# Kernel optimization log

Hardware: AMD Instinct MI355X
Metric: run time of the kernel (lower is better)

## Reference

```python
import jax, jax.numpy as jnp
import numpy as np

EMBED_DIM = 1024
NUM_HEADS = 16
HEAD_DIM = EMBED_DIM // NUM_HEADS
EPSILON = 1e-6
SCORE_SCALE = 1.0
B, L = 2, 2048


def setup_inputs() -> dict:
    key = jax.random.key(0)
    k0, k1, k2, k3, k4 = jax.random.split(key, 5)
    s_in = 1.0 / np.sqrt(EMBED_DIM)
    return {
        "x": jax.random.normal(k0, (B, L, EMBED_DIM), dtype=jnp.float32),
        "w_qkv": jax.random.normal(k1, (EMBED_DIM, 3 * EMBED_DIM), dtype=jnp.float32) * s_in,
        "b_qkv": jnp.zeros((3 * EMBED_DIM,), dtype=jnp.float32),
        "w_out": jax.random.normal(k2, (EMBED_DIM, EMBED_DIM), dtype=jnp.float32) * s_in,
        "b_out": jnp.zeros((EMBED_DIM,), dtype=jnp.float32),
    }


def reference(x, w_qkv, b_qkv, w_out, b_out):
    Bq, Lq, E = x.shape
    qkv = x @ w_qkv + b_qkv  # [B, L, 3E]
    q, k, v = jnp.split(qkv, 3, axis=-1)
    q = q.reshape(Bq, Lq, NUM_HEADS, HEAD_DIM).transpose(0, 2, 1, 3)  # bhld
    k = k.reshape(Bq, Lq, NUM_HEADS, HEAD_DIM).transpose(0, 2, 1, 3)
    v = v.reshape(Bq, Lq, NUM_HEADS, HEAD_DIM).transpose(0, 2, 1, 3)

    dot = jnp.einsum('bhid,bhjd->bhij', q, k)
    q_norm_sq = jnp.sum(q * q, axis=-1, keepdims=True)          # [b,h,L,1]
    k_norm_sq = jnp.sum(k * k, axis=-1, keepdims=True)          # [b,h,L,1]
    vals = q_norm_sq + k_norm_sq.transpose(0, 1, 3, 2)          # [b,h,L,L]
    scores = (dot * dot) / (vals - 2.0 * dot + EPSILON) * SCORE_SCALE

    mask = jnp.triu(jnp.ones((Lq, Lq), dtype=scores.dtype), k=1) * -1e9
    scores = scores + mask[None, None, :, :]
    attn = jax.nn.softmax(scores, axis=-1)
    out = jnp.einsum('bhij,bhjd->bhid', attn, v)
    out = out.transpose(0, 2, 1, 3).reshape(Bq, Lq, E)
    return out @ w_out + b_out
```

## Files before the change

kernel.cpp:

```cpp
#include <hip/hip_runtime.h>

#define EMBED 1024
#define NH 16
#define HD 64
#define SEQ 2048
#define BATCH 2
#define ROWS (BATCH*SEQ)
#define BHD (BATCH*NH)

typedef __bf16 bf16x8 __attribute__((ext_vector_type(8)));
typedef _Float16 f16x4 __attribute__((ext_vector_type(4)));
typedef float f32x4 __attribute__((ext_vector_type(4)));

__device__ __forceinline__ unsigned short f2bf(float f){
  union { float f; unsigned u; } v; v.f = f;
  unsigned r = v.u + 0x7fffu + ((v.u >> 16) & 1u);
  return (unsigned short)(r >> 16);
}
__device__ __forceinline__ float bf2f(unsigned short s){
  union { unsigned u; float f; } v; v.u = ((unsigned)s) << 16; return v.f;
}
__device__ __forceinline__ unsigned short f2h(float f){
  union { _Float16 h; unsigned short u; } v; v.h = (_Float16)f; return v.u;
}

typedef __attribute__((address_space(1))) unsigned int as1_t;
typedef __attribute__((address_space(3))) unsigned int as3_t;
__device__ __forceinline__ void async_ld16(const void* gp, void* lp){
  __builtin_amdgcn_global_load_lds((as1_t*)gp, (as3_t*)lp, 16, 0, 0);
}


__global__ __launch_bounds__(256) void k_prep(
    const float* __restrict__ x,     unsigned short* __restrict__ xb,
    const float* __restrict__ wqkv,  unsigned short* __restrict__ wqkvT,
    const float* __restrict__ wout,  unsigned short* __restrict__ woutT)
{
  __shared__ float t[32][33];
  int tid = threadIdx.x;
  int bx = blockIdx.x;
  if (bx < 4096){
    int i = bx*256 + tid;
    float4 f = ((const float4*)x)[i];
    ushort4 o; o.x=f2bf(f.x); o.y=f2bf(f.y); o.z=f2bf(f.z); o.w=f2bf(f.w);
    ((ushort4*)xb)[i] = o;
    return;
  }
  const float* in; unsigned short* out; int R, C, c0, r0;
  if (bx < 4096 + 3072){
    int bid = bx - 4096;
    in = wqkv; out = wqkvT; R = 1024; C = 3072;
    c0 = (bid % 96) * 32; r0 = (bid / 96) * 32;
  } else {
    int bid = bx - 7168;
    in = wout; out = woutT; R = 1024; C = 1024;
    c0 = (bid & 31) * 32; r0 = (bid >> 5) * 32;
  }
  int tx = tid & 31, ty = tid >> 5;
  #pragma unroll
  for (int i = 0; i < 4; i++){ int r = ty + i*8; t[r][tx] = in[(size_t)(r0+r)*C + c0 + tx]; }
  __syncthreads();
  #pragma unroll
  for (int i = 0; i < 4; i++){ int rr = ty + i*8; out[(size_t)(c0+rr)*R + r0 + tx] = f2bf(t[tx][rr]); }
}


__global__ __launch_bounds__(256) void k_gemm_qkv(
    const unsigned short* __restrict__ A,
    const unsigned short* __restrict__ BT,
    const float* __restrict__ bias,
    unsigned short* __restrict__ qo, unsigned short* __restrict__ ko,
    unsigned short* __restrict__ vT,
    float* __restrict__ qn, float* __restrict__ kn)
{
  __shared__ __align__(16) unsigned short As[128*32];
  __shared__ __align__(16) unsigned short Bs[128*32];
  const int K = EMBED;
  int m0 = blockIdx.x * 128, n0 = blockIdx.y * 128;
  int tid = threadIdx.x, lane = tid & 63, wave = tid >> 6;
  int wm = wave >> 1, wn = wave & 1;
  int l16 = lane & 15, quad = lane >> 4;
  f32x4 acc[4][4] = {};
  int c0i = wave*64 + lane, c1i = 256 + wave*64 + lane;
  int r0 = c0i >> 2, cc0 = (c0i & 3) * 8;
  int r1 = c1i >> 2, cc1 = (c1i & 3) * 8;
  unsigned short* lA0 = &As[(wave*64)*8];
  unsigned short* lA1 = &As[(256 + wave*64)*8];
  unsigned short* lB0 = &Bs[(wave*64)*8];
  unsigned short* lB1 = &Bs[(256 + wave*64)*8];
  for (int k0 = 0; k0 < K; k0 += 32){
    async_ld16((void*)&A [(size_t)(m0 + r0)*K + k0 + cc0], (void*)lA0);
    async_ld16((void*)&A [(size_t)(m0 + r1)*K + k0 + cc1], (void*)lA1);
    async_ld16((void*)&BT[(size_t)(n0 + r0)*K + k0 + cc0], (void*)lB0);
    async_ld16((void*)&BT[(size_t)(n0 + r1)*K + k0 + cc1], (void*)lB1);
    __syncthreads();
    bf16x8 af[4], bfr[4];
    #pragma unroll
    for (int mi = 0; mi < 4; mi++) af[mi]  = *(const bf16x8*)&As[(wm*64 + mi*16 + l16)*32 + quad*8];
    #pragma unroll
    for (int ni = 0; ni < 4; ni++) bfr[ni] = *(const bf16x8*)&Bs[(wn*64 + ni*16 + l16)*32 + quad*8];
    #pragma unroll
    for (int mi = 0; mi < 4; mi++)
      #pragma unroll
      for (int ni = 0; ni < 4; ni++)
        acc[mi][ni] = __builtin_amdgcn_mfma_f32_16x16x32_bf16(af[mi], bfr[ni], acc[mi][ni], 0, 0, 0);
    __syncthreads();
  }

  int which = n0 >> 10;
  int h = ((n0 & 1023) >> 6) + wn;
  if (which < 2){
    unsigned short* dst = (which == 0) ? qo : ko;
    float* ndst = (which == 0) ? qn : kn;
    #pragma unroll
    for (int mi = 0; mi < 4; mi++){
      float ns[4] = {0.f, 0.f, 0.f, 0.f};
      #pragma unroll
      for (int ni = 0; ni < 4; ni++)
        #pragma unroll
        for (int rr = 0; rr < 4; rr++){
          int row = m0 + wm*64 + mi*16 + quad*4 + rr;
          int col = n0 + wn*64 + ni*16 + l16;
          unsigned short bits = f2bf(acc[mi][ni][rr] + bias[col]);
          int b = row >> 11, l = row & 2047;
          dst[(((size_t)(b*NH + h))*SEQ + l)*HD + (col & 63)] = bits;
          float vq = bf2f(bits);
          ns[rr] += vq * vq;
        }
      #pragma unroll
      for (int rr = 0; rr < 4; rr++){
        float s = ns[rr];
        s += __shfl_xor(s, 1); s += __shfl_xor(s, 2);
        s += __shfl_xor(s, 4); s += __shfl_xor(s, 8);
        if (l16 == 0){
          int row = m0 + wm*64 + mi*16 + quad*4 + rr;
          int b = row >> 11, l = row & 2047;
          ndst[(size_t)(b*NH + h)*SEQ + l] = s;
        }
      }
    }
  } else {
    #pragma unroll
    for (int mi = 0; mi < 4; mi++)
      #pragma unroll
      for (int ni = 0; ni < 4; ni++){
        int row0 = m0 + wm*64 + mi*16 + quad*4;
        int col = n0 + wn*64 + ni*16 + l16;
        int b = row0 >> 11, l0 = row0 & 2047;
        ushort4 pk; unsigned short* pks = (unsigned short*)&pk;
        #pragma unroll
        for (int rr = 0; rr < 4; rr++)
          pks[rr] = f2h(acc[mi][ni][rr] + bias[col]);
        *(ushort4*)&vT[(((size_t)(b*NH + h))*HD + (col & 63))*SEQ + l0] = pk;
      }
  }
}


__global__ __launch_bounds__(128, 4) void k_attn(
    const unsigned short* __restrict__ qg,
    const unsigned short* __restrict__ kg,
    const unsigned short* __restrict__ vtg,
    const float* __restrict__ qn,
    const float* __restrict__ kn,
    float* __restrict__ Opart,
    float* __restrict__ Mp,
    float* __restrict__ Lp)
{
  __shared__ __align__(16) unsigned short Ks[2][32*72];
  __shared__ __align__(16) _Float16      Vs[2][64*36];
  int bh = blockIdx.y;
  int tid = threadIdx.x, lane = tid & 63, wave = tid >> 6;
  int l16 = lane & 15, quad = lane >> 4;
  int P = blockIdx.x >> 1, s = blockIdx.x & 1;

  const unsigned short* qbase = qg  + (size_t)bh * SEQ * HD;
  const unsigned short* kbase = kg  + (size_t)bh * SEQ * HD;
  const _Float16*       vtb   = (const _Float16*)vtg + (size_t)bh * HD * SEQ;
  const float* knb = kn + (size_t)bh * SEQ;

  int kd0 = tid >> 3,         kc0 = tid & 7;
  int kd1 = (tid + 128) >> 3, kc1 = tid & 7;
  int vd0 = tid >> 2,         vc0 = tid & 3;
  int vd1 = 32 + (tid >> 2),  vc1 = tid & 3;

  #pragma unroll
  for (int pass = 0; pass < 2; pass++){
    int t = pass ? (63 - P) : P;
    int nj = t + 1;
    int half = (nj + 1) >> 1;
    int jb_lo = s ? half : 0;
    int jb_hi = s ? nj : half;
    int q0 = t*32 + wave*16;

    bf16x8 aq[2];
    #pragma unroll
    for (int sk = 0; sk < 2; sk++)
      aq[sk] = *(const bf16x8*)&qbase[(size_t)(q0 + l16)*HD + sk*32 + quad*8];
    float qn_m = qn[(size_t)bh*SEQ + q0 + l16];

    float m_run = -1e30f, l_lane = 0.f;
    f32x4 oacc[4] = {};

    if (jb_lo < jb_hi){
      int jlo = jb_lo * 32;
      {
        uint4 ka = *(const uint4*)&kbase[(size_t)(jlo + kd0)*HD + kc0*8];
        uint4 kb = *(const uint4*)&kbase[(size_t)(jlo + kd1)*HD + kc1*8];
        uint4 va = *(const uint4*)&vtb[(size_t)vd0*SEQ + jlo + vc0*8];
        uint4 vb = *(const uint4*)&vtb[(size_t)vd1*SEQ + jlo + vc1*8];
        *(uint4*)&Ks[0][kd0*72 + kc0*8] = ka;
        *(uint4*)&Ks[0][kd1*72 + kc1*8] = kb;
        *(uint2*)&Vs[0][vd0*36 + vc0*8]     = make_uint2(va.x, va.y);
        *(uint2*)&Vs[0][vd0*36 + vc0*8 + 4] = make_uint2(va.z, va.w);
        *(uint2*)&Vs[0][vd1*36 + vc1*8]     = make_uint2(vb.x, vb.y);
        *(uint2*)&Vs[0][vd1*36 + vc1*8 + 4] = make_uint2(vb.z, vb.w);
      }
      __syncthreads();

      for (int jb = jb_lo; jb < jb_hi; jb++){
        int j0 = jb * 32;
        int buf = (jb - jb_lo) & 1;
        int jn = (jb + 1 < jb_hi) ? (jb + 1)*32 : j0;
        uint4 ka = *(const uint4*)&kbase[(size_t)(jn + kd0)*HD + kc0*8];
        uint4 kb = *(const uint4*)&kbase[(size_t)(jn + kd1)*HD + kc1*8];
        uint4 va = *(const uint4*)&vtb[(size_t)vd0*SEQ + jn + vc0*8];
        uint4 vb = *(const uint4*)&vtb[(size_t)vd1*SEQ + jn + vc1*8];

        f32x4 st[2] = {};
        #pragma unroll
        for (int tile = 0; tile < 2; tile++)
          #pragma unroll
          for (int sk = 0; sk < 2; sk++){
            bf16x8 ak = *(const bf16x8*)&Ks[buf][(tile*16 + l16)*72 + (sk*4 + quad)*8];
            st[tile] = __builtin_amdgcn_mfma_f32_16x16x32_bf16(ak, aq[sk], st[tile], 0, 0, 0);
          }
        float4 kn_a = *(const float4*)&knb[j0 + quad*4];
        float4 kn_b = *(const float4*)&knb[j0 + 16 + quad*4];
        float kn_j[2][4] = {{kn_a.x, kn_a.y, kn_a.z, kn_a.w}, {kn_b.x, kn_b.y, kn_b.z, kn_b.w}};
        int mg = q0 + l16;
        float sc[2][4];
        if (j0 + 32 > q0){
          #pragma unroll
          for (int tile = 0; tile < 2; tile++)
            #pragma unroll
            for (int rr = 0; rr < 4; rr++){
              int jg = j0 + tile*16 + quad*4 + rr;
              float dot = st[tile][rr];
              float den = fmaxf(qn_m + kn_j[tile][rr] - 2.0f*dot, 0.0f) + 1e-6f;
              float v = dot * dot * __builtin_amdgcn_rcpf(den);
              sc[tile][rr] = (jg <= mg) ? v : -1e30f;
            }
        } else {
          #pragma unroll
          for (int tile = 0; tile < 2; tile++)
            #pragma unroll
            for (int rr = 0; rr < 4; rr++){
              float dot = st[tile][rr];
              float den = fmaxf(qn_m + kn_j[tile][rr] - 2.0f*dot, 0.0f) + 1e-6f;
              sc[tile][rr] = dot * dot * __builtin_amdgcn_rcpf(den);
            }
        }
        float mx = fmaxf(fmaxf(fmaxf(sc[0][0], sc[0][1]), fmaxf(sc[0][2], sc[0][3])),
                         fmaxf(fmaxf(sc[1][0], sc[1][1]), fmaxf(sc[1][2], sc[1][3])));
        mx = fmaxf(mx, __shfl_xor(mx, 16));
        mx = fmaxf(mx, __shfl_xor(mx, 32));
        float mnew = fmaxf(m_run, mx);
        float alpha = __expf(m_run - mnew);
        m_run = mnew;

        float ps = 0.f;
        #pragma unroll
        for (int tile = 0; tile < 2; tile++)
          #pragma unroll
          for (int rr = 0; rr < 4; rr++){
            float e = __expf(sc[tile][rr] - mnew);
            sc[tile][rr] = e; ps += e;
          }
        l_lane = l_lane * alpha + ps;

        #pragma unroll
        for (int g = 0; g < 4; g++)
          #pragma unroll
          for (int rr = 0; rr < 4; rr++) oacc[g][rr] *= alpha;

        #pragma unroll
        for (int tile = 0; tile < 2; tile++){
          f16x4 pf;
          #pragma unroll
          for (int rr = 0; rr < 4; rr++) pf[rr] = (_Float16)sc[tile][rr];
          #pragma unroll
          for (int g = 0; g < 4; g++){
            f16x4 av = *(const f16x4*)&Vs[buf][(g*16 + l16)*36 + (tile*4 + quad)*4];
            oacc[g] = __builtin_amdgcn_mfma_f32_16x16x16f16(av, pf, oacc[g], 0, 0, 0);
          }
        }

        *(uint4*)&Ks[buf^1][kd0*72 + kc0*8] = ka;
        *(uint4*)&Ks[buf^1][kd1*72 + kc1*8] = kb;
        *(uint2*)&Vs[buf^1][vd0*36 + vc0*8]     = make_uint2(va.x, va.y);
        *(uint2*)&Vs[buf^1][vd0*36 + vc0*8 + 4] = make_uint2(va.z, va.w);
        *(uint2*)&Vs[buf^1][vd1*36 + vc1*8]     = make_uint2(vb.x, vb.y);
        *(uint2*)&Vs[buf^1][vd1*36 + vc1*8 + 4] = make_uint2(vb.z, vb.w);
        __syncthreads();
      }
    }

    float l_tot = l_lane + __shfl_xor(l_lane, 16);
    l_tot += __shfl_xor(l_tot, 32);

    int r = wave*16 + l16;
    size_t pb = ((size_t)(bh*64 + t)*2 + s) * (32*64);
    #pragma unroll
    for (int g = 0; g < 4; g++){
      float4 pk = make_float4(oacc[g][0], oacc[g][1], oacc[g][2], oacc[g][3]);
      *(float4*)&Opart[pb + (size_t)r*64 + g*16 + quad*4] = pk;
    }
    if (quad == 0){
      int mb = ((bh*64 + t)*2 + s)*32 + r;
      Mp[mb] = m_run;
      Lp[mb] = l_tot;
    }
    __syncthreads();
  }
}


__global__ __launch_bounds__(256) void k_combine(
    const float* __restrict__ Opart,
    const float* __restrict__ Mp,
    const float* __restrict__ Lp,
    unsigned short* __restrict__ attn_out)
{
  int t = blockIdx.x;
  int bh = blockIdx.y; int b = bh >> 4, h = bh & 15;
  int tid = threadIdx.x;
  int d = tid & 63, r8 = (tid >> 6) * 8;
  size_t i0 = ((size_t)(bh*64 + t)*2) * 2048;
  size_t i1 = i0 + 2048;
  int mb = ((bh*64 + t)*2) * 32;
  #pragma unroll
  for (int rr = 0; rr < 8; rr++){
    int r = r8 + rr;
    float m0 = Mp[mb + r],      m1 = Mp[mb + 32 + r];
    float l0 = Lp[mb + r],      l1 = Lp[mb + 32 + r];
    float ms = fmaxf(m0, m1);
    float w0 = __expf(m0 - ms), w1 = __expf(m1 - ms);
    float den = w0*l0 + w1*l1;
    float o = (w0*Opart[i0 + (size_t)r*64 + d] + w1*Opart[i1 + (size_t)r*64 + d]) / den;
    attn_out[(size_t)(b*SEQ + t*32 + r)*EMBED + h*HD + d] = f2bf(o);
  }
}


__global__ __launch_bounds__(256) void k_gemm_out(
    const unsigned short* __restrict__ A,
    const unsigned short* __restrict__ BT,
    const float* __restrict__ bias,
    float* __restrict__ out)
{
  __shared__ __align__(16) unsigned short As[128*32];
  __shared__ __align__(16) unsigned short Bs[128*32];
  const int K = EMBED;
  int m0 = blockIdx.x * 128, n0 = blockIdx.y * 128;
  int tid = threadIdx.x, lane = tid & 63, wave = tid >> 6;
  int wm = wave >> 1, wn = wave & 1;
  int l16 = lane & 15, quad = lane >> 4;
  f32x4 acc[4][4] = {};
  int c0i = wave*64 + lane, c1i = 256 + wave*64 + lane;
  int r0 = c0i >> 2, cc0 = (c0i & 3) * 8;
  int r1 = c1i >> 2, cc1 = (c1i & 3) * 8;
  unsigned short* lA0 = &As[(wave*64)*8];
  unsigned short* lA1 = &As[(256 + wave*64)*8];
  unsigned short* lB0 = &Bs[(wave*64)*8];
  unsigned short* lB1 = &Bs[(256 + wave*64)*8];
  for (int k0 = 0; k0 < K; k0 += 32){
    async_ld16((void*)&A [(size_t)(m0 + r0)*K + k0 + cc0], (void*)lA0);
    async_ld16((void*)&A [(size_t)(m0 + r1)*K + k0 + cc1], (void*)lA1);
    async_ld16((void*)&BT[(size_t)(n0 + r0)*K + k0 + cc0], (void*)lB0);
    async_ld16((void*)&BT[(size_t)(n0 + r1)*K + k0 + cc1], (void*)lB1);
    __syncthreads();
    bf16x8 af[4], bfr[4];
    #pragma unroll
    for (int mi = 0; mi < 4; mi++) af[mi]  = *(const bf16x8*)&As[(wm*64 + mi*16 + l16)*32 + quad*8];
    #pragma unroll
    for (int ni = 0; ni < 4; ni++) bfr[ni] = *(const bf16x8*)&Bs[(wn*64 + ni*16 + l16)*32 + quad*8];
    #pragma unroll
    for (int mi = 0; mi < 4; mi++)
      #pragma unroll
      for (int ni = 0; ni < 4; ni++)
        acc[mi][ni] = __builtin_amdgcn_mfma_f32_16x16x32_bf16(af[mi], bfr[ni], acc[mi][ni], 0, 0, 0);
    __syncthreads();
  }
  #pragma unroll
  for (int mi = 0; mi < 4; mi++)
    #pragma unroll
    for (int ni = 0; ni < 4; ni++)
      #pragma unroll
      for (int rr = 0; rr < 4; rr++){
        int row = m0 + wm*64 + mi*16 + quad*4 + rr;
        int col = n0 + wn*64 + ni*16 + l16;
        out[(size_t)row*EMBED + col] = acc[mi][ni][rr] + bias[col];
      }
}


extern "C" void kernel_launch(void* const* d_in, const int* in_sizes, int n_in,
                              void* d_out, int out_size, void* d_ws, size_t ws_size,
                              hipStream_t stream) {
  const float* x     = (const float*)d_in[0];
  const float* w_qkv = (const float*)d_in[1];
  const float* b_qkv = (const float*)d_in[2];
  const float* w_out = (const float*)d_in[3];
  const float* b_out = (const float*)d_in[4];
  float* out = (float*)d_out;

  char* ws = (char*)d_ws;
  size_t off = 0;
  auto alloc = [&](size_t bytes) -> void* {
    void* p = ws + off; off += (bytes + 255) & ~(size_t)255; return p;
  };
  unsigned short* xb    = (unsigned short*)alloc((size_t)ROWS * EMBED * 2);
  unsigned short* wqkvT = (unsigned short*)alloc((size_t)3 * EMBED * EMBED * 2);
  unsigned short* woutT = (unsigned short*)alloc((size_t)EMBED * EMBED * 2);
  unsigned short* qb    = (unsigned short*)alloc((size_t)ROWS * EMBED * 2);
  unsigned short* kb    = (unsigned short*)alloc((size_t)ROWS * EMBED * 2);
  unsigned short* vTb   = (unsigned short*)alloc((size_t)ROWS * EMBED * 2);
  float* qn = (float*)alloc((size_t)BHD * SEQ * 4);
  float* kn = (float*)alloc((size_t)BHD * SEQ * 4);
  float* Opart = (float*)alloc((size_t)BHD * 64 * 2 * 32 * 64 * 4);
  float* Mp    = (float*)alloc((size_t)BHD * 64 * 2 * 32 * 4);
  float* Lp    = (float*)alloc((size_t)BHD * 64 * 2 * 32 * 4);
  unsigned short* attnb = xb;

  k_prep<<<dim3(4096 + 3072 + 1024), dim3(256), 0, stream>>>(x, xb, w_qkv, wqkvT, w_out, woutT);
  k_gemm_qkv<<<dim3(ROWS/128, 3*EMBED/128), dim3(256), 0, stream>>>(xb, wqkvT, b_qkv, qb, kb, vTb, qn, kn);
  k_attn<<<dim3(64, BHD), dim3(128), 0, stream>>>(qb, kb, vTb, qn, kn, Opart, Mp, Lp);
  k_combine<<<dim3(64, BHD), dim3(256), 0, stream>>>(Opart, Mp, Lp, attnb);
  k_gemm_out<<<dim3(ROWS/128, EMBED/128), dim3(256), 0, stream>>>(attnb, woutT, b_out, out);
}
```

Before: 222.4 us.

## Recompute q norms in attention, store fp16 partials, shrink out-GEMM M tile

```diff
diff --git a/kernel.cpp b/kernel.cpp
--- a/kernel.cpp
+++ b/kernel.cpp
@@ -71,7 +71,7 @@
     const float* __restrict__ bias,
     unsigned short* __restrict__ qo, unsigned short* __restrict__ ko,
     unsigned short* __restrict__ vT,
-    float* __restrict__ qn, float* __restrict__ kn)
+    float* __restrict__ kn)
 {
   __shared__ __align__(16) unsigned short As[128*32];
   __shared__ __align__(16) unsigned short Bs[128*32];
@@ -109,9 +109,19 @@
 
   int which = n0 >> 10;
   int h = ((n0 & 1023) >> 6) + wn;
-  if (which < 2){
-    unsigned short* dst = (which == 0) ? qo : ko;
-    float* ndst = (which == 0) ? qn : kn;
+  if (which == 0){
+    #pragma unroll
+    for (int mi = 0; mi < 4; mi++)
+      #pragma unroll
+      for (int ni = 0; ni < 4; ni++)
+        #pragma unroll
+        for (int rr = 0; rr < 4; rr++){
+          int row = m0 + wm*64 + mi*16 + quad*4 + rr;
+          int col = n0 + wn*64 + ni*16 + l16;
+          int b = row >> 11, l = row & 2047;
+          qo[(((size_t)(b*NH + h))*SEQ + l)*HD + (col & 63)] = f2bf(acc[mi][ni][rr] + bias[col]);
+        }
+  } else if (which == 1){
     #pragma unroll
     for (int mi = 0; mi < 4; mi++){
       float ns[4] = {0.f, 0.f, 0.f, 0.f};
@@ -123,7 +133,7 @@
           int col = n0 + wn*64 + ni*16 + l16;
           unsigned short bits = f2bf(acc[mi][ni][rr] + bias[col]);
           int b = row >> 11, l = row & 2047;
-          dst[(((size_t)(b*NH + h))*SEQ + l)*HD + (col & 63)] = bits;
+          ko[(((size_t)(b*NH + h))*SEQ + l)*HD + (col & 63)] = bits;
           float vq = bf2f(bits);
           ns[rr] += vq * vq;
         }
@@ -135,7 +145,7 @@
         if (l16 == 0){
           int row = m0 + wm*64 + mi*16 + quad*4 + rr;
           int b = row >> 11, l = row & 2047;
-          ndst[(size_t)(b*NH + h)*SEQ + l] = s;
+          kn[(size_t)(b*NH + h)*SEQ + l] = s;
         }
       }
     }
@@ -161,9 +171,8 @@
     const unsigned short* __restrict__ qg,
     const unsigned short* __restrict__ kg,
     const unsigned short* __restrict__ vtg,
-    const float* __restrict__ qn,
     const float* __restrict__ kn,
-    float* __restrict__ Opart,
+    _Float16* __restrict__ Opart,
     float* __restrict__ Mp,
     float* __restrict__ Lp)
 {
@@ -197,7 +206,16 @@
     #pragma unroll
     for (int sk = 0; sk < 2; sk++)
       aq[sk] = *(const bf16x8*)&qbase[(size_t)(q0 + l16)*HD + sk*32 + quad*8];
-    float qn_m = qn[(size_t)bh*SEQ + q0 + l16];
+    float qn_lane = 0.f;
+    #pragma unroll
+    for (int sk = 0; sk < 2; sk++)
+      #pragma unroll
+      for (int i = 0; i < 8; i++){
+        float v = (float)aq[sk][i];
+        qn_lane += v * v;
+      }
+    float qn_m = qn_lane + __shfl_xor(qn_lane, 16);
+    qn_m += __shfl_xor(qn_m, 32);
 
     float m_run = -1e30f, l_lane = 0.f;
     f32x4 oacc[4] = {};
@@ -313,8 +331,10 @@
     size_t pb = ((size_t)(bh*64 + t)*2 + s) * (32*64);
     #pragma unroll
     for (int g = 0; g < 4; g++){
-      float4 pk = make_float4(oacc[g][0], oacc[g][1], oacc[g][2], oacc[g][3]);
-      *(float4*)&Opart[pb + (size_t)r*64 + g*16 + quad*4] = pk;
+      ushort4 pk;
+      pk.x = f2h(oacc[g][0]); pk.y = f2h(oacc[g][1]);
+      pk.z = f2h(oacc[g][2]); pk.w = f2h(oacc[g][3]);
+      *(ushort4*)&Opart[pb + (size_t)r*64 + g*16 + quad*4] = pk;
     }
     if (quad == 0){
       int mb = ((bh*64 + t)*2 + s)*32 + r;
@@ -327,7 +347,7 @@
 
 
 __global__ __launch_bounds__(256) void k_combine(
-    const float* __restrict__ Opart,
+    const _Float16* __restrict__ Opart,
     const float* __restrict__ Mp,
     const float* __restrict__ Lp,
     unsigned short* __restrict__ attn_out)
@@ -347,7 +367,7 @@
     float ms = fmaxf(m0, m1);
     float w0 = __expf(m0 - ms), w1 = __expf(m1 - ms);
     float den = w0*l0 + w1*l1;
-    float o = (w0*Opart[i0 + (size_t)r*64 + d] + w1*Opart[i1 + (size_t)r*64 + d]) / den;
+    float o = (w0*(float)Opart[i0 + (size_t)r*64 + d] + w1*(float)Opart[i1 + (size_t)r*64 + d]) / den;
     attn_out[(size_t)(b*SEQ + t*32 + r)*EMBED + h*HD + d] = f2bf(o);
   }
 }
@@ -359,46 +379,45 @@
     const float* __restrict__ bias,
     float* __restrict__ out)
 {
-  __shared__ __align__(16) unsigned short As[128*32];
+  __shared__ __align__(16) unsigned short As[64*32];
   __shared__ __align__(16) unsigned short Bs[128*32];
   const int K = EMBED;
-  int m0 = blockIdx.x * 128, n0 = blockIdx.y * 128;
+  int m0 = blockIdx.x * 64, n0 = blockIdx.y * 128;
   int tid = threadIdx.x, lane = tid & 63, wave = tid >> 6;
   int wm = wave >> 1, wn = wave & 1;
   int l16 = lane & 15, quad = lane >> 4;
-  f32x4 acc[4][4] = {};
+  f32x4 acc[2][4] = {};
+  int ra = tid >> 2, ca = (tid & 3) * 8;
   int c0i = wave*64 + lane, c1i = 256 + wave*64 + lane;
-  int r0 = c0i >> 2, cc0 = (c0i & 3) * 8;
-  int r1 = c1i >> 2, cc1 = (c1i & 3) * 8;
-  unsigned short* lA0 = &As[(wave*64)*8];
-  unsigned short* lA1 = &As[(256 + wave*64)*8];
+  int rb0 = c0i >> 2, cb0 = (c0i & 3) * 8;
+  int rb1 = c1i >> 2, cb1 = (c1i & 3) * 8;
+  unsigned short* lA  = &As[(wave*64)*8];
   unsigned short* lB0 = &Bs[(wave*64)*8];
   unsigned short* lB1 = &Bs[(256 + wave*64)*8];
   for (int k0 = 0; k0 < K; k0 += 32){
-    async_ld16((void*)&A [(size_t)(m0 + r0)*K + k0 + cc0], (void*)lA0);
-    async_ld16((void*)&A [(size_t)(m0 + r1)*K + k0 + cc1], (void*)lA1);
-    async_ld16((void*)&BT[(size_t)(n0 + r0)*K + k0 + cc0], (void*)lB0);
-    async_ld16((void*)&BT[(size_t)(n0 + r1)*K + k0 + cc1], (void*)lB1);
+    async_ld16((void*)&A [(size_t)(m0 + ra)*K + k0 + ca],   (void*)lA);
+    async_ld16((void*)&BT[(size_t)(n0 + rb0)*K + k0 + cb0], (void*)lB0);
+    async_ld16((void*)&BT[(size_t)(n0 + rb1)*K + k0 + cb1], (void*)lB1);
     __syncthreads();
-    bf16x8 af[4], bfr[4];
-    #pragma unroll
-    for (int mi = 0; mi < 4; mi++) af[mi]  = *(const bf16x8*)&As[(wm*64 + mi*16 + l16)*32 + quad*8];
+    bf16x8 af[2], bfr[4];
+    #pragma unroll
+    for (int mi = 0; mi < 2; mi++) af[mi]  = *(const bf16x8*)&As[(wm*32 + mi*16 + l16)*32 + quad*8];
     #pragma unroll
     for (int ni = 0; ni < 4; ni++) bfr[ni] = *(const bf16x8*)&Bs[(wn*64 + ni*16 + l16)*32 + quad*8];
     #pragma unroll
-    for (int mi = 0; mi < 4; mi++)
+    for (int mi = 0; mi < 2; mi++)
       #pragma unroll
       for (int ni = 0; ni < 4; ni++)
         acc[mi][ni] = __builtin_amdgcn_mfma_f32_16x16x32_bf16(af[mi], bfr[ni], acc[mi][ni], 0, 0, 0);
     __syncthreads();
   }
   #pragma unroll
-  for (int mi = 0; mi < 4; mi++)
+  for (int mi = 0; mi < 2; mi++)
     #pragma unroll
     for (int ni = 0; ni < 4; ni++)
       #pragma unroll
       for (int rr = 0; rr < 4; rr++){
-        int row = m0 + wm*64 + mi*16 + quad*4 + rr;
+        int row = m0 + wm*32 + mi*16 + quad*4 + rr;
         int col = n0 + wn*64 + ni*16 + l16;
         out[(size_t)row*EMBED + col] = acc[mi][ni][rr] + bias[col];
       }
@@ -426,16 +445,15 @@
   unsigned short* qb    = (unsigned short*)alloc((size_t)ROWS * EMBED * 2);
   unsigned short* kb    = (unsigned short*)alloc((size_t)ROWS * EMBED * 2);
   unsigned short* vTb   = (unsigned short*)alloc((size_t)ROWS * EMBED * 2);
-  float* qn = (float*)alloc((size_t)BHD * SEQ * 4);
   float* kn = (float*)alloc((size_t)BHD * SEQ * 4);
-  float* Opart = (float*)alloc((size_t)BHD * 64 * 2 * 32 * 64 * 4);
+  _Float16* Opart = (_Float16*)alloc((size_t)BHD * 64 * 2 * 32 * 64 * 2);
   float* Mp    = (float*)alloc((size_t)BHD * 64 * 2 * 32 * 4);
   float* Lp    = (float*)alloc((size_t)BHD * 64 * 2 * 32 * 4);
   unsigned short* attnb = xb;
 
   k_prep<<<dim3(4096 + 3072 + 1024), dim3(256), 0, stream>>>(x, xb, w_qkv, wqkvT, w_out, woutT);
-  k_gemm_qkv<<<dim3(ROWS/128, 3*EMBED/128), dim3(256), 0, stream>>>(xb, wqkvT, b_qkv, qb, kb, vTb, qn, kn);
-  k_attn<<<dim3(64, BHD), dim3(128), 0, stream>>>(qb, kb, vTb, qn, kn, Opart, Mp, Lp);
+  k_gemm_qkv<<<dim3(ROWS/128, 3*EMBED/128), dim3(256), 0, stream>>>(xb, wqkvT, b_qkv, qb, kb, vTb, kn);
+  k_attn<<<dim3(64, BHD), dim3(128), 0, stream>>>(qb, kb, vTb, kn, Opart, Mp, Lp);
   k_combine<<<dim3(64, BHD), dim3(256), 0, stream>>>(Opart, Mp, Lp, attnb);
-  k_gemm_out<<<dim3(ROWS/128, EMBED/128), dim3(256), 0, stream>>>(attnb, woutT, b_out, out);
-}
+  k_gemm_out<<<dim3(ROWS/64, EMBED/128), dim3(256), 0, stream>>>(attnb, woutT, b_out, out);
+}
```

Result: no change. 218.8 us (-1.6%).
